# Performance work log

Hardware: AMD Instinct MI355X
Metric: run time of the kernel (lower is better)

Reference implementation:

```python
import jax, jax.numpy as jnp
import numpy as np

N = 100000
E = 3200000
IN_DIM = 512
HID = 256
NUM_CLASSES = 16
P_DROP = 0.5
EPS_BN = 1e-5


def setup_inputs() -> dict:
    key = jax.random.key(0)
    ks = jax.random.split(key, 6)
    x = jax.random.normal(ks[0], (N, IN_DIM), jnp.float32)
    edge_src = jax.random.randint(ks[1], (E,), 0, N, dtype=jnp.int32)
    edge_dst = jax.random.randint(ks[2], (E,), 0, N, dtype=jnp.int32)
    # Glorot-ish init for GraphConv weights (bias=False in the module)
    W1 = jax.random.normal(ks[3], (IN_DIM, HID), jnp.float32) / np.sqrt(IN_DIM).astype(np.float32)
    W2 = jax.random.normal(ks[4], (HID, NUM_CLASSES), jnp.float32) / np.sqrt(HID).astype(np.float32)
    W3 = jax.random.normal(ks[5], (HID, NUM_CLASSES), jnp.float32) / np.sqrt(HID).astype(np.float32)
    return {"x": x, "W1": W1, "W2": W2, "W3": W3,
            "edge_src": edge_src, "edge_dst": edge_dst}


def _graph_conv(h, W, edge_src, edge_dst, out_inv_sqrt, in_inv_sqrt):
    # DGL GraphConv, norm='both', bias=False:
    #   rst = D_in^{-1/2} * A_agg( D_out^{-1/2} * h @ W )
    # Apply W before aggregation (out_dim <= in_dim here); same math as DGL.
    h = h * out_inv_sqrt[:, None]          # [N, d_in]
    h = h @ W                              # [N, d_out]
    agg = jax.ops.segment_sum(h[edge_src], edge_dst, num_segments=h.shape[0])
    return agg * in_inv_sqrt[:, None]


def _dropout(key, x, p=P_DROP):
    keep = jax.random.bernoulli(key, 1.0 - p, x.shape)
    return jnp.where(keep, x / (1.0 - p), jnp.zeros((), x.dtype))


def reference(x, W1, W2, W3, edge_src, edge_dst):
    n = x.shape[0]
    ones = jnp.ones(edge_src.shape[0], x.dtype)
    out_deg = jax.ops.segment_sum(ones, edge_src, num_segments=n)
    in_deg = jax.ops.segment_sum(ones, edge_dst, num_segments=n)
    out_is = jnp.maximum(out_deg, 1.0) ** -0.5   # DGL clamps degree to min 1
    in_is = jnp.maximum(in_deg, 1.0) ** -0.5

    k1, k2a, k2b, keps = jax.random.split(jax.random.key(42), 4)

    # gc1 + relu
    h = _dropout(k1, x)
    h = jax.nn.relu(_graph_conv(h, W1, edge_src, edge_dst, out_is, in_is))

    # BatchNorm1d(affine=False, track_running_stats=False): batch stats
    mean = jnp.mean(h, axis=0)
    var = jnp.var(h, axis=0)
    h = (h - mean) * jax.lax.rsqrt(var + EPS_BN)

    # gc2 (mu) and gc3 (logvar), each with its own dropout of hidden1
    mu = _graph_conv(_dropout(k2a, h), W2, edge_src, edge_dst, out_is, in_is)
    logvar = _graph_conv(_dropout(k2b, h), W3, edge_src, edge_dst, out_is, in_is)

    # reparameterize (training): eps * exp(logvar) + mu  (note: exp(logvar), per source)
    eps = jax.random.normal(keps, mu.shape, mu.dtype)
    return eps * jnp.exp(logvar) + mu
```

## Files before the change

### kernel.cpp

```cpp
#include <hip/hip_runtime.h>
#include <stdint.h>

#define N_NODES 100000
#define N_EDGES 3200000
#define IN_DIM  512
#define HID     256
#define NCLS    16

#define DBLK   256
#define DCHUNK (N_EDGES / DBLK)
#define DWIN2  50000

typedef unsigned short u16;
typedef __attribute__((ext_vector_type(8))) short short8;
typedef __attribute__((ext_vector_type(4))) float float4v;

__device__ __forceinline__ float bf2f(u16 u) {
  return __uint_as_float(((uint32_t)u) << 16);
}
__device__ __forceinline__ u16 f2bf(float f) {
  uint32_t u = __float_as_uint(f);
  return (u16)((u + 0x7fffu + ((u >> 16) & 1u)) >> 16);
}
__device__ __forceinline__ void acc8(float* a, uint4 v) {
  a[0] += bf2f((u16)(v.x & 0xffffu)); a[1] += bf2f((u16)(v.x >> 16));
  a[2] += bf2f((u16)(v.y & 0xffffu)); a[3] += bf2f((u16)(v.y >> 16));
  a[4] += bf2f((u16)(v.z & 0xffffu)); a[5] += bf2f((u16)(v.z >> 16));
  a[6] += bf2f((u16)(v.w & 0xffffu)); a[7] += bf2f((u16)(v.w >> 16));
}

__host__ __device__ __forceinline__ uint32_t rotl32(uint32_t v, int d) {
  return (v << d) | (v >> (32 - d));
}

__host__ __device__ __forceinline__ void threefry2x32(uint32_t k0, uint32_t k1,
    uint32_t x0, uint32_t x1, uint32_t& o0, uint32_t& o1) {
  uint32_t ks0 = k0, ks1 = k1, ks2 = k0 ^ k1 ^ 0x1BD11BDAu;
  x0 += ks0; x1 += ks1;
#define TF_R(r) { x0 += x1; x1 = rotl32(x1, r); x1 ^= x0; }
  TF_R(13) TF_R(15) TF_R(26) TF_R(6)
  x0 += ks1; x1 += ks2 + 1u;
  TF_R(17) TF_R(29) TF_R(16) TF_R(24)
  x0 += ks2; x1 += ks0 + 2u;
  TF_R(13) TF_R(15) TF_R(26) TF_R(6)
  x0 += ks0; x1 += ks1 + 3u;
  TF_R(17) TF_R(29) TF_R(16) TF_R(24)
  x0 += ks1; x1 += ks2 + 4u;
  TF_R(13) TF_R(15) TF_R(26) TF_R(6)
  x0 += ks2; x1 += ks0 + 5u;
#undef TF_R
  o0 = x0; o1 = x1;
}

__host__ __device__ __forceinline__ uint32_t tf_bits32(uint32_t k0, uint32_t k1, uint32_t idx) {
  uint32_t o0, o1;
  threefry2x32(k0, k1, 0u, idx, o0, o1);
  return o0 ^ o1;
}

__device__ __forceinline__ float erfinv_f32(float x) {
  float w = -log1pf(-x * x);
  float p;
  if (w < 5.0f) {
    w -= 2.5f;
    p = 2.81022636e-08f;
    p = fmaf(p, w, 3.43273939e-07f);
    p = fmaf(p, w, -3.5233877e-06f);
    p = fmaf(p, w, -4.39150654e-06f);
    p = fmaf(p, w, 0.00021858087f);
    p = fmaf(p, w, -0.00125372503f);
    p = fmaf(p, w, -0.00417768164f);
    p = fmaf(p, w, 0.246640727f);
    p = fmaf(p, w, 1.50140941f);
  } else {
    w = sqrtf(w) - 3.0f;
    p = -0.000200214257f;
    p = fmaf(p, w, 0.000100950558f);
    p = fmaf(p, w, 0.00134934322f);
    p = fmaf(p, w, -0.00367342844f);
    p = fmaf(p, w, 0.00573950773f);
    p = fmaf(p, w, -0.0076224613f);
    p = fmaf(p, w, 0.00943887047f);
    p = fmaf(p, w, 1.00167406f);
    p = fmaf(p, w, 2.83297682f);
  }
  return p * x;
}

__global__ __launch_bounds__(1024) void hist_k(
    const int* __restrict__ esrc, const int* __restrict__ edst,
    u16* __restrict__ P16) {
  __shared__ uint32_t h32[DWIN2 / 2];
  const int b = blockIdx.x, tid = threadIdx.x;
  const int ebase = b * DCHUNK;
  for (int w = 0; w < 2; ++w) {
    const int lo = w * DWIN2;
    for (int i = tid; i < DWIN2 / 2; i += 1024) h32[i] = 0u;
    __syncthreads();
    for (int e = ebase + tid; e < ebase + DCHUNK; e += 1024) {
      int s = esrc[e], d = edst[e];
      unsigned su = (unsigned)(s - lo);
      if (su < (unsigned)DWIN2) atomicAdd(&h32[su >> 1], 1u << ((su & 1) * 16));
      unsigned du = (unsigned)(d - lo);
      if (du < (unsigned)DWIN2) atomicAdd(&h32[du >> 1], 0x100u << ((du & 1) * 16));
    }
    __syncthreads();
    for (int i = tid; i < DWIN2 / 2; i += 1024) {
      *(uint32_t*)(P16 + (size_t)b * N_NODES + lo + 2 * i) = h32[i];
    }
    __syncthreads();
  }
}

__global__ void degsum_k(u16* __restrict__ P16, int* __restrict__ ind,
                         float* __restrict__ out_is, float* __restrict__ in_is) {
  int n = blockIdx.x * 256 + threadIdx.x;
  if (n >= N_NODES) return;
  uint32_t to = 0, ti = 0;
#pragma unroll 8
  for (int b = 0; b < DBLK; ++b) {
    uint32_t v = P16[(size_t)b * N_NODES + n];
    P16[(size_t)b * N_NODES + n] = (u16)ti;
    to += v & 0xffu; ti += v >> 8;
  }
  ind[n] = (int)ti;
  out_is[n] = rsqrtf(fmaxf((float)to, 1.0f));
  in_is[n]  = rsqrtf(fmaxf((float)ti, 1.0f));
}

__global__ __launch_bounds__(1024) void scan_offsets_k(
    const int* __restrict__ ind, int* __restrict__ row_ofs) {
  __shared__ int wsum[16];
  const int tid = threadIdx.x;
  const int lane = tid & 63, wv = tid >> 6;
  int running = 0;
  for (int base = 0; base < N_NODES; base += 1024) {
    const int i = base + tid;
    int v = (i < N_NODES) ? ind[i] : 0;
    int sc = v;
#pragma unroll
    for (int d = 1; d < 64; d <<= 1) {
      int t = __shfl_up(sc, d, 64);
      if (lane >= d) sc += t;
    }
    if (lane == 63) wsum[wv] = sc;
    __syncthreads();
    if (wv == 0) {
      int t = (lane < 16) ? wsum[lane] : 0;
#pragma unroll
      for (int d = 1; d < 16; d <<= 1) {
        int u = __shfl_up(t, d, 64);
        if (lane >= d) t += u;
      }
      if (lane < 16) wsum[lane] = t;
    }
    __syncthreads();
    int wbase = (wv > 0) ? wsum[wv - 1] : 0;
    if (i < N_NODES) row_ofs[i] = running + wbase + sc - v;
    running += wsum[15];
    __syncthreads();
  }
  if (tid == 0) row_ofs[N_NODES] = running;
}

__global__ __launch_bounds__(1024) void place_k(
    const int* __restrict__ esrc, const int* __restrict__ edst,
    const u16* __restrict__ P16, const int* __restrict__ row_ofs,
    int* __restrict__ csr) {
  __shared__ uint32_t cur32[N_NODES / 4];
  const int b = blockIdx.x, tid = threadIdx.x;
  for (int i = tid; i < N_NODES / 4; i += 1024) cur32[i] = 0u;
  __syncthreads();
  const int ebase = b * DCHUNK;
  for (int e = ebase + tid; e < ebase + DCHUNK; e += 1024) {
    int d = edst[e];
    int base = row_ofs[d] + (int)P16[(size_t)b * N_NODES + d];
    uint32_t old = atomicAdd(&cur32[d >> 2], 1u << ((d & 3) * 8));
    int c = (int)((old >> ((d & 3) * 8)) & 0xffu);
    csr[base + c] = esrc[e];
  }
}

__global__ void gen_mask2_k(uint32_t ka0, uint32_t ka1, uint32_t kb0, uint32_t kb1,
                            uint32_t* __restrict__ maska, uint32_t* __restrict__ maskb) {
  uint32_t idx = blockIdx.x * blockDim.x + threadIdx.x;
  uint32_t ba = tf_bits32(ka0, ka1, idx);
  uint32_t bb = tf_bits32(kb0, kb1, idx);
  unsigned long long bala = __ballot((ba >> 31) == 0u);
  unsigned long long balb = __ballot((bb >> 31) == 0u);
  if ((threadIdx.x & 63) == 0) {
    uint32_t w = idx >> 5;
    maska[w] = (uint32_t)bala;
    maska[w + 1] = (uint32_t)(bala >> 32);
    maskb[w] = (uint32_t)balb;
    maskb[w + 1] = (uint32_t)(balb >> 32);
  }
}

__global__ __launch_bounds__(256) void cast_x_k(
    const float* __restrict__ x, const float* __restrict__ out_is,
    uint32_t k0, uint32_t k1, u16* __restrict__ Xb) {
  uint32_t t = blockIdx.x * 256u + threadIdx.x;
  uint32_t idx = t * 8u;
  uint32_t row = idx >> 9;
  float sc = 2.0f * out_is[row];
  float4 v0 = *(const float4*)(x + idx);
  float4 v1 = *(const float4*)(x + idx + 4);
  float vv[8] = {v0.x, v0.y, v0.z, v0.w, v1.x, v1.y, v1.z, v1.w};
  u16 o[8];
#pragma unroll
  for (int j = 0; j < 8; ++j) {
    uint32_t bits = tf_bits32(k0, k1, idx + (uint32_t)j);
    float val = (bits >> 31) ? 0.0f : vv[j] * sc;
    o[j] = f2bf(val);
  }
  uint4 pk;
  pk.x = (uint32_t)o[0] | ((uint32_t)o[1] << 16);
  pk.y = (uint32_t)o[2] | ((uint32_t)o[3] << 16);
  pk.z = (uint32_t)o[4] | ((uint32_t)o[5] << 16);
  pk.w = (uint32_t)o[6] | ((uint32_t)o[7] << 16);
  *(uint4*)(Xb + idx) = pk;
}

__global__ void cast_w1_k(const float* __restrict__ W1, u16* __restrict__ W1t) {
  int idx = blockIdx.x * blockDim.x + threadIdx.x;
  int k = idx >> 8, n = idx & 255;
  W1t[n * IN_DIM + k] = f2bf(W1[idx]);
}

__global__ void cast_w23_k(const float* __restrict__ W2, const float* __restrict__ W3,
                           u16* __restrict__ Wt23) {
  int idx = blockIdx.x * blockDim.x + threadIdx.x;
  int n = idx >> 8, k = idx & 255;
  float v = (n < 16) ? W2[k * NCLS + n] : W3[k * NCLS + (n - 16)];
  Wt23[n * HID + k] = f2bf(v);
}

#define LDA 40
__global__ __launch_bounds__(256) void gemm1_k(
    const u16* __restrict__ Xb, const u16* __restrict__ W1t, u16* __restrict__ X1b) {
  __shared__ u16 As[64 * LDA];
  __shared__ u16 Bs[256 * LDA];
  const int tid = threadIdx.x;
  const int w = tid >> 6, l = tid & 63;
  const int m16 = l & 15, q = l >> 4;
  const long base_row = (long)blockIdx.x * 64;

  float4v acc[4][4];
#pragma unroll
  for (int i = 0; i < 4; ++i)
#pragma unroll
    for (int j = 0; j < 4; ++j) acc[i][j] = (float4v)0.0f;

  const int arow = tid >> 2, ac = tid & 3;
  const long agr = base_row + arow;

  for (int k0 = 0; k0 < IN_DIM; k0 += 32) {
    uint4 va = make_uint4(0, 0, 0, 0);
    if (agr < N_NODES) va = *(const uint4*)(Xb + agr * IN_DIM + k0 + ac * 8);
    *(uint4*)(As + arow * LDA + ac * 8) = va;
#pragma unroll
    for (int c = 0; c < 4; ++c) {
      uint4 vb = *(const uint4*)(W1t + (size_t)tid * IN_DIM + k0 + c * 8);
      *(uint4*)(Bs + tid * LDA + c * 8) = vb;
    }
    __syncthreads();
    short8 a[4], b[4];
#pragma unroll
    for (int rt = 0; rt < 4; ++rt)
      a[rt] = *(const short8*)(As + (rt * 16 + m16) * LDA + q * 8);
#pragma unroll
    for (int ct = 0; ct < 4; ++ct)
      b[ct] = *(const short8*)(Bs + ((w * 4 + ct) * 16 + m16) * LDA + q * 8);
#pragma unroll
    for (int rt = 0; rt < 4; ++rt)
#pragma unroll
      for (int ct = 0; ct < 4; ++ct)
        acc[rt][ct] = __builtin_amdgcn_mfma_f32_16x16x32_bf16(a[rt], b[ct], acc[rt][ct], 0, 0, 0);
    __syncthreads();
  }
#pragma unroll
  for (int rt = 0; rt < 4; ++rt) {
#pragma unroll
    for (int r = 0; r < 4; ++r) {
      long grow = base_row + rt * 16 + q * 4 + r;
      if (grow < N_NODES) {
#pragma unroll
        for (int ct = 0; ct < 4; ++ct)
          X1b[grow * HID + (w * 4 + ct) * 16 + m16] = f2bf(acc[rt][ct][r]);
      }
    }
  }
}

__global__ __launch_bounds__(256) void agg_relu_k(
    const u16* __restrict__ X1b, const int* __restrict__ row_ofs,
    const int* __restrict__ csr, const float* __restrict__ in_is,
    u16* __restrict__ h1b) {
  int d = blockIdx.x * 4 + (threadIdx.x >> 6);
  int lane = threadIdx.x & 63;
  int half = lane >> 5;
  int col = (lane & 31) * 8;
  int beg = row_ofs[d], end = row_ofs[d + 1];
  float a[8];
#pragma unroll
  for (int i = 0; i < 8; ++i) a[i] = 0.0f;
  int j = beg + half;
  for (; j + 14 < end; j += 16) {
    int s0 = csr[j],      s1 = csr[j + 2],  s2 = csr[j + 4],  s3 = csr[j + 6];
    int s4 = csr[j + 8],  s5 = csr[j + 10], s6 = csr[j + 12], s7 = csr[j + 14];
    uint4 v0 = *(const uint4*)(X1b + (size_t)s0 * HID + col);
    uint4 v1 = *(const uint4*)(X1b + (size_t)s1 * HID + col);
    uint4 v2 = *(const uint4*)(X1b + (size_t)s2 * HID + col);
    uint4 v3 = *(const uint4*)(X1b + (size_t)s3 * HID + col);
    uint4 v4 = *(const uint4*)(X1b + (size_t)s4 * HID + col);
    uint4 v5 = *(const uint4*)(X1b + (size_t)s5 * HID + col);
    uint4 v6 = *(const uint4*)(X1b + (size_t)s6 * HID + col);
    uint4 v7 = *(const uint4*)(X1b + (size_t)s7 * HID + col);
    acc8(a, v0); acc8(a, v1); acc8(a, v2); acc8(a, v3);
    acc8(a, v4); acc8(a, v5); acc8(a, v6); acc8(a, v7);
  }
  for (; j + 6 < end; j += 8) {
    int s0 = csr[j], s1 = csr[j + 2], s2 = csr[j + 4], s3 = csr[j + 6];
    uint4 v0 = *(const uint4*)(X1b + (size_t)s0 * HID + col);
    uint4 v1 = *(const uint4*)(X1b + (size_t)s1 * HID + col);
    uint4 v2 = *(const uint4*)(X1b + (size_t)s2 * HID + col);
    uint4 v3 = *(const uint4*)(X1b + (size_t)s3 * HID + col);
    acc8(a, v0); acc8(a, v1); acc8(a, v2); acc8(a, v3);
  }
  for (; j < end; j += 2) {
    uint4 v0 = *(const uint4*)(X1b + (size_t)csr[j] * HID + col);
    acc8(a, v0);
  }
#pragma unroll
  for (int i = 0; i < 8; ++i) a[i] += __shfl(a[i], lane ^ 32, 64);
  if (half == 0) {
    float is = in_is[d];
    u16 o[8];
#pragma unroll
    for (int i = 0; i < 8; ++i) o[i] = f2bf(fmaxf(a[i] * is, 0.0f));
    uint4 pk;
    pk.x = (uint32_t)o[0] | ((uint32_t)o[1] << 16);
    pk.y = (uint32_t)o[2] | ((uint32_t)o[3] << 16);
    pk.z = (uint32_t)o[4] | ((uint32_t)o[5] << 16);
    pk.w = (uint32_t)o[6] | ((uint32_t)o[7] << 16);
    *(uint4*)(h1b + (size_t)d * HID + col) = pk;
  }
}

__global__ __launch_bounds__(256) void bn_stats_k(const u16* __restrict__ h1b,
                                                  float* __restrict__ bn) {
  __shared__ float ls[512];
  const int tid = threadIdx.x;
  const int cb = (tid & 31) * 8;
  const int ms = tid >> 5;
  float s[8], s2[8];
#pragma unroll
  for (int i = 0; i < 8; ++i) { s[i] = 0.f; s2[i] = 0.f; }
  for (int m = ms;; m += 8) {
    int r = blockIdx.x + 256 * m;
    if (r >= N_NODES) break;
    uint4 v = *(const uint4*)(h1b + (size_t)r * HID + cb);
    float f[8];
    f[0] = bf2f((u16)(v.x & 0xffffu)); f[1] = bf2f((u16)(v.x >> 16));
    f[2] = bf2f((u16)(v.y & 0xffffu)); f[3] = bf2f((u16)(v.y >> 16));
    f[4] = bf2f((u16)(v.z & 0xffffu)); f[5] = bf2f((u16)(v.z >> 16));
    f[6] = bf2f((u16)(v.w & 0xffffu)); f[7] = bf2f((u16)(v.w >> 16));
#pragma unroll
    for (int i = 0; i < 8; ++i) { s[i] += f[i]; s2[i] += f[i] * f[i]; }
  }
  ls[tid] = 0.f; ls[tid + 256] = 0.f;
  __syncthreads();
#pragma unroll
  for (int i = 0; i < 8; ++i) {
    atomicAdd(&ls[cb + i], s[i]);
    atomicAdd(&ls[256 + cb + i], s2[i]);
  }
  __syncthreads();
  atomicAdd(&bn[tid], ls[tid]);
  atomicAdd(&bn[HID + tid], ls[256 + tid]);
}

__global__ void bn_fin_k(float* __restrict__ bn) {
  int c = threadIdx.x;
  float mean = bn[c] / (float)N_NODES;
  float var = bn[HID + c] / (float)N_NODES - mean * mean;
  float istd = rsqrtf(var + 1e-5f);
  bn[512 + c] = istd;
  bn[768 + c] = -mean * istd;
}

#define WLS 264
__global__ __launch_bounds__(256) void gemm23_k(
    const u16* __restrict__ h1b, const u16* __restrict__ Wt23,
    const uint32_t* __restrict__ mask2a, const uint32_t* __restrict__ mask2b,
    const float* __restrict__ out_is, const float* __restrict__ bn,
    u16* __restrict__ XMLV) {
  __shared__ u16 Wls[32 * WLS];
  __shared__ float cB[HID], cA[HID];
  const int tid = threadIdx.x;
#pragma unroll
  for (int i = 0; i < 4; ++i) {
    int idx = tid + i * 256;
    int n = idx >> 5, c = idx & 31;
    *(uint4*)(Wls + n * WLS + c * 8) = ((const uint4*)Wt23)[idx];
  }
  cB[tid] = bn[512 + tid];
  cA[tid] = bn[768 + tid];
  __syncthreads();

  const int wv = tid >> 6, lane = tid & 63;
  const int m = lane & 15, q = lane >> 4;
  const long arow = (long)blockIdx.x * 64 + wv * 16 + m;
  const bool valid = arow < N_NODES;
  const float osc = valid ? 2.0f * out_is[arow] : 0.0f;

  float4v accM = (float4v)0.0f, accL = (float4v)0.0f;
  for (int kc = 0; kc < HID; kc += 32) {
    const int kof = kc + q * 8;
    uint4 hv = make_uint4(0, 0, 0, 0);
    uint32_t wa = 0, wb = 0;
    if (valid) {
      hv = *(const uint4*)(h1b + arow * HID + kof);
      uint32_t widx = ((uint32_t)arow * HID + (uint32_t)kc) >> 5;
      wa = mask2a[widx] >> (q * 8);
      wb = mask2b[widx] >> (q * 8);
    }
    float4 B0 = *(const float4*)(cB + kof);
    float4 B1 = *(const float4*)(cB + kof + 4);
    float4 A0 = *(const float4*)(cA + kof);
    float4 A1 = *(const float4*)(cA + kof + 4);
    float hval[8] = {
      bf2f((u16)(hv.x & 0xffffu)), bf2f((u16)(hv.x >> 16)),
      bf2f((u16)(hv.y & 0xffffu)), bf2f((u16)(hv.y >> 16)),
      bf2f((u16)(hv.z & 0xffffu)), bf2f((u16)(hv.z >> 16)),
      bf2f((u16)(hv.w & 0xffffu)), bf2f((u16)(hv.w >> 16))};
    float nb[8] = {B0.x, B0.y, B0.z, B0.w, B1.x, B1.y, B1.z, B1.w};
    float na[8] = {A0.x, A0.y, A0.z, A0.w, A1.x, A1.y, A1.z, A1.w};
    short8 Aa, Ab;
#pragma unroll
    for (int jj = 0; jj < 8; ++jj) {
      float t = fmaf(hval[jj], nb[jj], na[jj]) * osc;
      u16 tb = f2bf(t);
      Aa[jj] = (short)(((wa >> jj) & 1u) ? tb : 0);
      Ab[jj] = (short)(((wb >> jj) & 1u) ? tb : 0);
    }
    short8 Bm = *(const short8*)(Wls + m * WLS + kof);
    short8 Bl = *(const short8*)(Wls + (16 + m) * WLS + kof);
    accM = __builtin_amdgcn_mfma_f32_16x16x32_bf16(Aa, Bm, accM, 0, 0, 0);
    accL = __builtin_amdgcn_mfma_f32_16x16x32_bf16(Ab, Bl, accL, 0, 0, 0);
  }
#pragma unroll
  for (int r = 0; r < 4; ++r) {
    long srow = (long)blockIdx.x * 64 + wv * 16 + q * 4 + r;
    if (srow < N_NODES) {
      XMLV[srow * 32 + m]      = f2bf(accM[r]);
      XMLV[srow * 32 + 16 + m] = f2bf(accL[r]);
    }
  }
}

__global__ __launch_bounds__(256) void agg_final_k(
    const u16* __restrict__ XMLV, const int* __restrict__ row_ofs,
    const int* __restrict__ csr, const float* __restrict__ in_is,
    uint32_t ke0, uint32_t ke1, float* __restrict__ out) {
  int g = blockIdx.x * 4 + (threadIdx.x >> 6);
  int lane = threadIdx.x & 63;
  int half = lane >> 5, c = lane & 31;
  int beg = row_ofs[g], end = row_ofs[g + 1];
  float s = 0.f;
  int j = beg + half;
  for (; j + 14 < end; j += 16) {
    int s0 = csr[j],      s1 = csr[j + 2],  s2 = csr[j + 4],  s3 = csr[j + 6];
    int s4 = csr[j + 8],  s5 = csr[j + 10], s6 = csr[j + 12], s7 = csr[j + 14];
    float v0 = bf2f(XMLV[(size_t)s0 * 32 + c]);
    float v1 = bf2f(XMLV[(size_t)s1 * 32 + c]);
    float v2 = bf2f(XMLV[(size_t)s2 * 32 + c]);
    float v3 = bf2f(XMLV[(size_t)s3 * 32 + c]);
    float v4 = bf2f(XMLV[(size_t)s4 * 32 + c]);
    float v5 = bf2f(XMLV[(size_t)s5 * 32 + c]);
    float v6 = bf2f(XMLV[(size_t)s6 * 32 + c]);
    float v7 = bf2f(XMLV[(size_t)s7 * 32 + c]);
    s += v0; s += v1; s += v2; s += v3;
    s += v4; s += v5; s += v6; s += v7;
  }
  for (; j + 6 < end; j += 8) {
    int s0 = csr[j], s1 = csr[j + 2], s2 = csr[j + 4], s3 = csr[j + 6];
    float v0 = bf2f(XMLV[(size_t)s0 * 32 + c]);
    float v1 = bf2f(XMLV[(size_t)s1 * 32 + c]);
    float v2 = bf2f(XMLV[(size_t)s2 * 32 + c]);
    float v3 = bf2f(XMLV[(size_t)s3 * 32 + c]);
    s += v0; s += v1; s += v2; s += v3;
  }
  for (; j < end; j += 2) s += bf2f(XMLV[(size_t)csr[j] * 32 + c]);
  s += __shfl(s, lane ^ 32, 64);
  if (half == 0) {
    s *= in_is[g];
    float other = __shfl(s, lane ^ 16, 64);
    if (c < 16) {
      uint32_t i = (uint32_t)(g * NCLS + c);
      uint32_t bits = tf_bits32(ke0, ke1, i);
      float f = __uint_as_float((bits >> 9) | 0x3f800000u) - 1.0f;
      const float lo = -0.99999994f;
      float u = fmaxf(lo, fmaf(f, 2.0f, lo));
      float eps = 1.41421356f * erfinv_f32(u);
      out[i] = eps * expf(other) + s;
    }
  }
}

extern "C" void kernel_launch(void* const* d_in, const int* in_sizes, int n_in,
                              void* d_out, int out_size, void* d_ws, size_t ws_size,
                              hipStream_t stream) {
  (void)in_sizes; (void)n_in; (void)out_size; (void)ws_size;
  const float* x  = (const float*)d_in[0];
  const float* W1 = (const float*)d_in[1];
  const float* W2 = (const float*)d_in[2];
  const float* W3 = (const float*)d_in[3];
  const int* esrc = (const int*)d_in[4];
  const int* edst = (const int*)d_in[5];
  float* out = (float*)d_out;

  uint32_t kb[8];
  for (int j = 0; j < 4; ++j)
    threefry2x32(0u, 42u, 0u, (uint32_t)j, kb[2 * j], kb[2 * j + 1]);

  char* p = (char*)d_ws;
  auto take = [&](size_t bytes) -> void* {
    void* r = (void*)p;
    p += (bytes + 255) & ~(size_t)255;
    return r;
  };
  u16* Xb        = (u16*)take(sizeof(u16) * (size_t)N_NODES * IN_DIM);
  u16* X1b       = (u16*)take(sizeof(u16) * (size_t)N_NODES * HID);
  u16* h1b       = (u16*)take(sizeof(u16) * (size_t)N_NODES * HID);
  u16* XMLV      = (u16*)take(sizeof(u16) * (size_t)N_NODES * 32);
  u16* W1t       = (u16*)take(sizeof(u16) * (size_t)IN_DIM * HID);
  u16* Wt23      = (u16*)take(sizeof(u16) * 32 * HID);
  uint32_t* mask2a = (uint32_t*)take((size_t)N_NODES * HID / 8);
  uint32_t* mask2b = (uint32_t*)take((size_t)N_NODES * HID / 8);
  int* in_deg    = (int*)take(sizeof(int) * N_NODES);
  float* out_is  = (float*)take(sizeof(float) * N_NODES);
  float* in_is   = (float*)take(sizeof(float) * N_NODES);
  int* row_ofs   = (int*)take(sizeof(int) * (N_NODES + 1));
  int* csr       = (int*)take(sizeof(int) * N_EDGES);
  float* bn      = (float*)take(sizeof(float) * 1024);

  u16* P16 = (u16*)Xb;

  hipMemsetAsync(bn, 0, sizeof(float) * 512, stream);

  hist_k<<<DBLK, 1024, 0, stream>>>(esrc, edst, P16);
  degsum_k<<<(N_NODES + 255) / 256, 256, 0, stream>>>(P16, in_deg, out_is, in_is);
  scan_offsets_k<<<1, 1024, 0, stream>>>(in_deg, row_ofs);
  place_k<<<DBLK, 1024, 0, stream>>>(esrc, edst, P16, row_ofs, csr);

  gen_mask2_k<<<(N_NODES * HID) / 256, 256, 0, stream>>>(kb[2], kb[3], kb[4], kb[5],
                                                         mask2a, mask2b);

  cast_w1_k<<<(IN_DIM * HID) / 256, 256, 0, stream>>>(W1, W1t);
  cast_w23_k<<<(32 * HID) / 256, 256, 0, stream>>>(W2, W3, Wt23);
  cast_x_k<<<(N_NODES * IN_DIM / 8) / 256, 256, 0, stream>>>(x, out_is, kb[0], kb[1], Xb);

  gemm1_k<<<(N_NODES + 63) / 64, 256, 0, stream>>>(Xb, W1t, X1b);
  agg_relu_k<<<N_NODES / 4, 256, 0, stream>>>(X1b, row_ofs, csr, in_is, h1b);
  bn_stats_k<<<256, 256, 0, stream>>>(h1b, bn);
  bn_fin_k<<<1, 256, 0, stream>>>(bn);
  gemm23_k<<<(N_NODES + 63) / 64, 256, 0, stream>>>(h1b, Wt23, mask2a, mask2b, out_is, bn, XMLV);
  agg_final_k<<<N_NODES / 4, 256, 0, stream>>>(XMLV, row_ofs, csr, in_is, kb[6], kb[7], out);
}
```

Baseline: 1.034 ms.

## Rework first GEMM with direct-to-LDS loads, swizzled shared tiles and larger blocks

```diff
diff --git a/kernel.cpp b/kernel.cpp
--- a/kernel.cpp
+++ b/kernel.cpp
@@ -27,6 +27,12 @@
   a[2] += bf2f((u16)(v.y & 0xffffu)); a[3] += bf2f((u16)(v.y >> 16));
   a[4] += bf2f((u16)(v.z & 0xffffu)); a[5] += bf2f((u16)(v.z >> 16));
   a[6] += bf2f((u16)(v.w & 0xffffu)); a[7] += bf2f((u16)(v.w >> 16));
+}
+
+__device__ __forceinline__ void gload16(const void* g, void* l) {
+  __builtin_amdgcn_global_load_lds(
+      (const __attribute__((address_space(1))) uint32_t*)g,
+      (__attribute__((address_space(3))) uint32_t*)l, 16, 0, 0);
 }
 
 __host__ __device__ __forceinline__ uint32_t rotl32(uint32_t v, int d) {
@@ -222,29 +228,33 @@
   *(uint4*)(Xb + idx) = pk;
 }
 
-__global__ void cast_w1_k(const float* __restrict__ W1, u16* __restrict__ W1t) {
+__global__ void cast_w_k(const float* __restrict__ W1, const float* __restrict__ W2,
+                         const float* __restrict__ W3, u16* __restrict__ W1t,
+                         u16* __restrict__ Wt23) {
   int idx = blockIdx.x * blockDim.x + threadIdx.x;
-  int k = idx >> 8, n = idx & 255;
-  W1t[n * IN_DIM + k] = f2bf(W1[idx]);
-}
-
-__global__ void cast_w23_k(const float* __restrict__ W2, const float* __restrict__ W3,
-                           u16* __restrict__ Wt23) {
-  int idx = blockIdx.x * blockDim.x + threadIdx.x;
-  int n = idx >> 8, k = idx & 255;
-  float v = (n < 16) ? W2[k * NCLS + n] : W3[k * NCLS + (n - 16)];
-  Wt23[n * HID + k] = f2bf(v);
-}
-
-#define LDA 40
-__global__ __launch_bounds__(256) void gemm1_k(
+  if (idx < IN_DIM * HID) {
+    int k = idx >> 8, n = idx & 255;
+    W1t[n * IN_DIM + k] = f2bf(W1[idx]);
+  } else {
+    int t = idx - IN_DIM * HID;
+    int n = t >> 8, k = t & 255;
+    float v = (n < 16) ? W2[k * NCLS + n] : W3[k * NCLS + (n - 16)];
+    Wt23[n * HID + k] = f2bf(v);
+  }
+}
+
+#define G1_BM 128
+#define G1_BKC 8
+__global__ __launch_bounds__(512, 2) void gemm1_k(
     const u16* __restrict__ Xb, const u16* __restrict__ W1t, u16* __restrict__ X1b) {
-  __shared__ u16 As[64 * LDA];
-  __shared__ u16 Bs[256 * LDA];
+  __shared__ u16 As[G1_BM * 64];
+  __shared__ u16 Bs[256 * 64];
   const int tid = threadIdx.x;
-  const int w = tid >> 6, l = tid & 63;
-  const int m16 = l & 15, q = l >> 4;
-  const long base_row = (long)blockIdx.x * 64;
+  const int wid = tid >> 6, lane = tid & 63;
+  const int wr = wid >> 2, wc = wid & 3;
+  const int m16 = lane & 15, q = lane >> 4;
+  const int srow = lane >> 3, schunk = lane & 7;
+  const long base_row = (long)blockIdx.x * G1_BM;
 
   float4v acc[4][4];
 #pragma unroll
@@ -252,42 +262,54 @@
 #pragma unroll
     for (int j = 0; j < 4; ++j) acc[i][j] = (float4v)0.0f;
 
-  const int arow = tid >> 2, ac = tid & 3;
-  const long agr = base_row + arow;
-
-  for (int k0 = 0; k0 < IN_DIM; k0 += 32) {
-    uint4 va = make_uint4(0, 0, 0, 0);
-    if (agr < N_NODES) va = *(const uint4*)(Xb + agr * IN_DIM + k0 + ac * 8);
-    *(uint4*)(As + arow * LDA + ac * 8) = va;
-#pragma unroll
-    for (int c = 0; c < 4; ++c) {
-      uint4 vb = *(const uint4*)(W1t + (size_t)tid * IN_DIM + k0 + c * 8);
-      *(uint4*)(Bs + tid * LDA + c * 8) = vb;
-    }
-    __syncthreads();
-    short8 a[4], b[4];
-#pragma unroll
-    for (int rt = 0; rt < 4; ++rt)
-      a[rt] = *(const short8*)(As + (rt * 16 + m16) * LDA + q * 8);
-#pragma unroll
-    for (int ct = 0; ct < 4; ++ct)
-      b[ct] = *(const short8*)(Bs + ((w * 4 + ct) * 16 + m16) * LDA + q * 8);
-#pragma unroll
-    for (int rt = 0; rt < 4; ++rt)
-#pragma unroll
-      for (int ct = 0; ct < 4; ++ct)
-        acc[rt][ct] = __builtin_amdgcn_mfma_f32_16x16x32_bf16(a[rt], b[ct], acc[rt][ct], 0, 0, 0);
+  for (int ks = 0; ks < IN_DIM / 64; ++ks) {
+#pragma unroll
+    for (int i = 0; i < 2; ++i) {
+      int j = wid * 2 + i;
+      int row = j * 8 + srow;
+      int gch = ks * G1_BKC + (schunk ^ (row & 7));
+      gload16(Xb + (base_row + row) * IN_DIM + gch * 8, As + j * 512);
+    }
+#pragma unroll
+    for (int i = 0; i < 4; ++i) {
+      int j = wid * 4 + i;
+      int n = j * 8 + srow;
+      int gch = ks * G1_BKC + (schunk ^ (n & 7));
+      gload16(W1t + (size_t)n * IN_DIM + gch * 8, Bs + j * 512);
+    }
+    __syncthreads();
+#pragma unroll
+    for (int kk = 0; kk < 2; ++kk) {
+      short8 a[4], b[4];
+      const int kq = kk * 4 + q;
+      const int c = kq ^ (m16 & 7);
+#pragma unroll
+      for (int rt = 0; rt < 4; ++rt) {
+        int row = wr * 64 + rt * 16 + m16;
+        a[rt] = *(const short8*)(As + row * 64 + c * 8);
+      }
+#pragma unroll
+      for (int ct = 0; ct < 4; ++ct) {
+        int n = wc * 64 + ct * 16 + m16;
+        b[ct] = *(const short8*)(Bs + n * 64 + c * 8);
+      }
+#pragma unroll
+      for (int rt = 0; rt < 4; ++rt)
+#pragma unroll
+        for (int ct = 0; ct < 4; ++ct)
+          acc[rt][ct] = __builtin_amdgcn_mfma_f32_16x16x32_bf16(a[rt], b[ct], acc[rt][ct], 0, 0, 0);
+    }
     __syncthreads();
   }
 #pragma unroll
   for (int rt = 0; rt < 4; ++rt) {
 #pragma unroll
     for (int r = 0; r < 4; ++r) {
-      long grow = base_row + rt * 16 + q * 4 + r;
+      long grow = base_row + wr * 64 + rt * 16 + q * 4 + r;
       if (grow < N_NODES) {
 #pragma unroll
         for (int ct = 0; ct < 4; ++ct)
-          X1b[grow * HID + (w * 4 + ct) * 16 + m16] = f2bf(acc[rt][ct][r]);
+          X1b[grow * HID + wc * 64 + ct * 16 + m16] = f2bf(acc[rt][ct][r]);
       }
     }
   }
@@ -484,15 +506,11 @@
     s += v0; s += v1; s += v2; s += v3;
     s += v4; s += v5; s += v6; s += v7;
   }
-  for (; j + 6 < end; j += 8) {
-    int s0 = csr[j], s1 = csr[j + 2], s2 = csr[j + 4], s3 = csr[j + 6];
-    float v0 = bf2f(XMLV[(size_t)s0 * 32 + c]);
-    float v1 = bf2f(XMLV[(size_t)s1 * 32 + c]);
-    float v2 = bf2f(XMLV[(size_t)s2 * 32 + c]);
-    float v3 = bf2f(XMLV[(size_t)s3 * 32 + c]);
-    s += v0; s += v1; s += v2; s += v3;
-  }
-  for (; j < end; j += 2) s += bf2f(XMLV[(size_t)csr[j] * 32 + c]);
+#pragma unroll
+  for (int k = 0; k < 8; ++k) {
+    int e = j + 2 * k;
+    if (e < end) s += bf2f(XMLV[(size_t)csr[e] * 32 + c]);
+  }
   s += __shfl(s, lane ^ 32, 64);
   if (half == 0) {
     s *= in_is[g];
@@ -558,11 +576,10 @@
   gen_mask2_k<<<(N_NODES * HID) / 256, 256, 0, stream>>>(kb[2], kb[3], kb[4], kb[5],
                                                          mask2a, mask2b);
 
-  cast_w1_k<<<(IN_DIM * HID) / 256, 256, 0, stream>>>(W1, W1t);
-  cast_w23_k<<<(32 * HID) / 256, 256, 0, stream>>>(W2, W3, Wt23);
+  cast_w_k<<<(IN_DIM * HID + 32 * HID) / 256, 256, 0, stream>>>(W1, W2, W3, W1t, Wt23);
   cast_x_k<<<(N_NODES * IN_DIM / 8) / 256, 256, 0, stream>>>(x, out_is, kb[0], kb[1], Xb);
 
-  gemm1_k<<<(N_NODES + 63) / 64, 256, 0, stream>>>(Xb, W1t, X1b);
+  gemm1_k<<<(N_NODES + G1_BM - 1) / G1_BM, 512, 0, stream>>>(Xb, W1t, X1b);
   agg_relu_k<<<N_NODES / 4, 256, 0, stream>>>(X1b, row_ofs, csr, in_is, h1b);
   bn_stats_k<<<256, 256, 0, stream>>>(h1b, bn);
   bn_fin_k<<<1, 256, 0, stream>>>(bn);
```

Result: no change. 1.015 ms (-1.9%).
